# Kernel optimization log

Measured on AMD Instinct MI355X. Metric: run time of the kernel, lower is better.

## Reference

```python
import jax, jax.numpy as jnp
import numpy as np

# ---- constants ----
RC = 6.0            # radial cutoff for Bessel basis
SQ2 = 1.4142135623730951
SQ3 = 1.7320508075688772
SQ6 = 2.449489742783178
CY2 = 2.7386127875258306  # sqrt(15/2), l=2 spherical-harmonic norm
G, N_NODES, N_EDGES = 4, 4096, 65536
NB, C, NZ = 8, 32, 3

# orthonormal basis of symmetric-traceless 3x3 matrices <-> 5-vector (real l=2)

def t5_from_mat(S):
    r2, r6 = 1.0 / SQ2, 1.0 / SQ6
    a = (S[..., 0, 1] + S[..., 1, 0]) * r2
    b = (S[..., 1, 2] + S[..., 2, 1]) * r2
    c = (2.0 * S[..., 2, 2] - S[..., 0, 0] - S[..., 1, 1]) * r6
    d = (S[..., 0, 2] + S[..., 2, 0]) * r2
    e = (S[..., 0, 0] - S[..., 1, 1]) * r2
    return jnp.stack([a, b, c, d, e], axis=-1)

def mat_from_t5(t):
    r2, r6 = 1.0 / SQ2, 1.0 / SQ6
    a, b, c, d, e = (t[..., i] for i in range(5))
    Sxx = -c * r6 + e * r2
    Syy = -c * r6 - e * r2
    Szz = 2.0 * c * r6
    Sxy, Syz, Sxz = a * r2, b * r2, d * r2
    row0 = jnp.stack([Sxx, Sxy, Sxz], -1)
    row1 = jnp.stack([Sxy, Syy, Syz], -1)
    row2 = jnp.stack([Sxz, Syz, Szz], -1)
    return jnp.stack([row0, row1, row2], -2)

def bessel(r, nbessel):
    # sqrt(2/rc) * sin(n*pi*r/rc) / r, smooth at r=0 via sinc
    n = jnp.arange(1, nbessel + 1, dtype=r.dtype)
    x = r[..., None] * n / RC
    return jnp.sqrt(2.0 / RC) * (n * jnp.pi / RC) * jnp.sinc(x)

def sph(vec):
    # real spherical harmonics l=0,1,2 of the unit edge vector
    u = vec / (jnp.linalg.norm(vec, axis=-1, keepdims=True) + 1e-9)
    Y0 = jnp.ones(u.shape[:-1] + (1,), u.dtype)
    Y1 = SQ3 * u
    outer = u[..., :, None] * u[..., None, :]
    Y2 = CY2 * t5_from_mat(outer - jnp.eye(3, dtype=u.dtype) / 3.0)
    return Y0, Y1, Y2

def message_pass(r, vec, h_scalar, src, dst, Wrad, n_nodes):
    # A_l[n] = sum_{e: dst(e)=n} R(r_e)W_l * h_src[e] * Y_l(v_e)
    R = bessel(r, Wrad.shape[0])                      # [E, nb]
    w = jnp.einsum('eb,bcl->ecl', R, Wrad)            # [E, C, 3]
    Y0, Y1, Y2 = sph(vec)
    hs = h_scalar[src]                                # gather -> [E, C]
    m0 = (w[:, :, 0] * hs)[:, :, None] * Y0[:, None, :]
    m1 = (w[:, :, 1] * hs)[:, :, None] * Y1[:, None, :]
    m2 = (w[:, :, 2] * hs)[:, :, None] * Y2[:, None, :]
    m = jnp.concatenate([m0, m1, m2], axis=-1)        # [E, C, 9]
    A = jax.ops.segment_sum(m, dst, num_segments=n_nodes)
    return A[..., 0], A[..., 1:4], A[..., 4:9]        # [N,C],[N,C,3],[N,C,5]

def prod3body(A0, A1, A2, Wp):
    # symmetric 3-body tensor product A x A with CG paths to 0e+1o+2e
    dot11 = jnp.sum(A1 * A1, -1)
    dot22 = jnp.sum(A2 * A2, -1)
    B0 = Wp[0] * A0 * A0 + Wp[1] * dot11 + Wp[2] * dot22
    T = mat_from_t5(A2)                               # [N,C,3,3]
    Tv = jnp.einsum('ncij,ncj->nci', T, A1)           # 1x2 -> 1 path
    B1 = Wp[3][:, None] * A0[..., None] * A1 + Wp[4][:, None] * Tv
    eye = jnp.eye(3, dtype=A1.dtype)
    S = A1[..., :, None] * A1[..., None, :] - (dot11 / 3.0)[..., None, None] * eye
    B2 = Wp[5][:, None] * A0[..., None] * A2 + Wp[6][:, None] * t5_from_mat(S)
    return B0, B1, B2

def readout_l2(B0, B2, Wr0, Wr2):
    # per-node symmetric 3x3: isotropic scalar part + traceless l=2 part
    s = B0 @ Wr0                                      # [N]
    t = jnp.einsum('ncm,c->nm', B2, Wr2)              # [N,5]
    eye = jnp.eye(3, dtype=B0.dtype)
    return s[:, None, None] * eye / SQ3 + mat_from_t5(t)


def setup_inputs() -> dict:
    key = jax.random.key(0)
    ks = jax.random.split(key, 14)
    sc = 1.0 / np.sqrt(C)
    return {
        'x': jax.random.uniform(ks[0], (G, N_EDGES), jnp.float32),
        'x_v': jax.random.normal(ks[1], (G, N_EDGES, 3), jnp.float32),
        'node_attr': jax.random.uniform(ks[2], (G, N_NODES, NZ), jnp.float32),
        'edge_index': jax.random.randint(ks[3], (G, 2, N_EDGES), 0, N_NODES),
        'Wz': jax.random.normal(ks[4], (NZ, C), jnp.float32) * 0.5,
        'Wrad1': jax.random.normal(ks[5], (NB, C, 3), jnp.float32) * 0.5,
        'Wrad2': jax.random.normal(ks[6], (NB, C, 3), jnp.float32) * 0.5,
        'Wp': jax.random.normal(ks[7], (7, C), jnp.float32) * 0.5,
        'Wr0_1': jax.random.normal(ks[8], (C,), jnp.float32) * sc,
        'Wr2_1': jax.random.normal(ks[9], (C,), jnp.float32) * sc,
        'Wm0': jax.random.normal(ks[10], (C, C), jnp.float32) * sc,
        'Wr0_2': jax.random.normal(ks[11], (C,), jnp.float32) * sc,
        'Wr2_2': jax.random.normal(ks[12], (C,), jnp.float32) * sc,
    }


def reference(x, x_v, node_attr, edge_index, Wz, Wrad1, Wrad2, Wp,
              Wr0_1, Wr2_1, Wm0, Wr0_2, Wr2_2):
    n_nodes = node_attr.shape[1]

    def per_graph(r, vec, na, ei):
        src, dst = ei[0], ei[1]
        h0 = na @ Wz                                  # NodeFeaturesStart
        A0, A1, A2 = message_pass(r, vec, h0, src, dst, Wrad1, n_nodes)
        B0, B1, B2 = prod3body(A0, A1, A2, Wp)
        M1 = readout_l2(B0, B2, Wr0_1, Wr2_1)         # [N,3,3]
        f0 = jax.nn.silu(B0 @ Wm0)                    # updated node scalars
        A0b, A1b, A2b = message_pass(r, vec, f0, src, dst, Wrad2, n_nodes)
        C0, C1, C2b = prod3body(A0b, A1b, A2b, Wp)    # prod reused (as in torch code)
        M2 = readout_l2(C0, C2b, Wr0_2, Wr2_2)
        return M1.sum(0) + M2.sum(0)                  # [3,3]

    return jax.vmap(per_graph)(x, x_v, node_attr, edge_index)
```

## Files before the change

### kernel.cpp

```cpp
#include <hip/hip_runtime.h>
#include <hip/hip_fp16.h>
#include <math.h>

#define G_ 4
#define N_ 4096
#define E_ 65536
#define NB_ 8
#define C_ 32
#define CAP_ 48

typedef _Float16 h2 __attribute__((ext_vector_type(2)));

__device__ __forceinline__ float red32(float v) {
    #pragma unroll
    for (int o = 16; o >= 1; o >>= 1) v += __shfl_xor(v, o, 32);
    return v;
}

__device__ __forceinline__ float pack2f(float a, float b) {
    union { __half2 h; unsigned u; } cvt;
    cvt.h = __floats2half2_rn(a, b);
    return __uint_as_float(cvt.u);
}

__device__ __forceinline__ unsigned pack2u(float a, float b) {
    union { __half2 h; unsigned u; } cvt;
    cvt.h = __floats2half2_rn(a, b);
    return cvt.u;
}

__device__ __forceinline__ h2 as_h2(float fbits) {
    union { float f; h2 h; } u; u.f = fbits; return u.h;
}

__device__ __forceinline__ h2 as_h2u(unsigned ubits) {
    union { unsigned u; h2 h; } u2; u2.u = ubits; return u2.h;
}

__global__ void k_prep(const float* __restrict__ x, const float* __restrict__ xv,
                       const int* __restrict__ ei, const float* __restrict__ na,
                       const float* __restrict__ Wz, const float* __restrict__ Wrad1,
                       const float* __restrict__ Wrad2, int* __restrict__ cur,
                       float4* __restrict__ rec32, float* __restrict__ h,
                       unsigned* __restrict__ Wpk) {
    int idx = blockIdx.x * 256 + threadIdx.x;

    if (blockIdx.x == 0 && threadIdx.x < 192) {
        int t = threadIdx.x;
        int pass = t / 96, rem = t % 96;
        int c = rem / 3, l = rem % 3;
        const float* W = pass ? Wrad2 : Wrad1;
        unsigned* dst = Wpk + ((size_t)(pass * C_ + c) * 3 + l) * 4;
        #pragma unroll
        for (int j = 0; j < 4; ++j)
            dst[j] = pack2u(W[(2 * j) * (C_ * 3) + c * 3 + l],
                            W[(2 * j + 1) * (C_ * 3) + c * 3 + l]);
    }

    #pragma unroll
    for (int t = 0; t < 2; ++t) {
        int hidx = idx + t * (G_ * E_);
        int c = hidx & (C_ - 1), gn = hidx >> 5;
        const float* a = na + (size_t)gn * 3;
        h[hidx] = a[0] * Wz[c] + a[1] * Wz[C_ + c] + a[2] * Wz[2 * C_ + c];
    }

    int g = idx >> 16, e = idx & (E_ - 1);
    const int* eib = ei + (size_t)g * 2 * E_;
    int src = eib[e], dst = eib[E_ + e];
    int local = atomicAdd(&cur[g * N_ + dst], 1);
    if (local >= CAP_) return;
    size_t slot = (size_t)(g * N_ + dst) * CAP_ + local;

    float r = x[idx];
    const float SQ2RC = 0.57735026918962576f;
    const float K1 = 0.5235987755982988f;
    float rinv = (r > 1e-12f) ? (1.0f / r) : 0.0f;
    bool  tiny = (r <= 1e-12f);
    float xx = K1 * r;
    float s1, c1;
    __sincosf(xx, &s1, &c1);
    float twoc = 2.0f * c1;
    float R[NB_];
    float sm = 0.f, sn = s1;
    #pragma unroll
    for (int n = 1; n <= NB_; ++n) {
        R[n - 1] = tiny ? (SQ2RC * K1 * (float)n) : (SQ2RC * sn * rinv);
        float nx = twoc * sn - sm;
        sm = sn; sn = nx;
    }

    float ax = xv[(size_t)idx * 3 + 0];
    float ay = xv[(size_t)idx * 3 + 1];
    float az = xv[(size_t)idx * 3 + 2];
    float inr = 1.7320508075688772f * rsqrtf(ax * ax + ay * ay + az * az + 1e-18f);

    float4* p = rec32 + slot * 2;
    p[0] = make_float4(ax * inr, ay * inr, az * inr, __int_as_float(src));
    p[1] = make_float4(pack2f(R[0], R[1]), pack2f(R[2], R[3]),
                       pack2f(R[4], R[5]), pack2f(R[6], R[7]));
}

template <int PASS>
__global__ void __launch_bounds__(256) k_node(
        const float4* __restrict__ rec32, const int* __restrict__ cur,
        const float* __restrict__ hin, const unsigned* __restrict__ Wpk,
        const float* __restrict__ Wp, const float* __restrict__ Wr0,
        const float* __restrict__ Wr2, const float* __restrict__ Wm0,
        float* __restrict__ f0out, float* __restrict__ pacc) {
    __shared__ float4 sbin[4][CAP_ * 2];
    __shared__ float  sred[6][4][32];
    int tid  = threadIdx.x;
    int wv   = tid >> 6;
    int lane = tid & 63;
    int c    = lane & 31;
    int eo   = lane >> 5;
    int gn   = blockIdx.x * 4 + wv;
    int g    = gn >> 12;

    const uint4* wp = (const uint4*)(Wpk + (size_t)((PASS - 1) * C_ + c) * 12);
    uint4 wq0 = wp[0], wq1 = wp[1], wq2 = wp[2];

    int deg = cur[gn];
    if (deg > CAP_) deg = CAP_;
    {
        const float4* bin = rec32 + (size_t)gn * CAP_ * 2;
        int nf4 = deg * 2;
        for (int j = lane; j < nf4; j += 64) sbin[wv][j] = bin[j];
    }
    __syncthreads();

    h2 wh[3][4];
    wh[0][0] = as_h2u(wq0.x); wh[0][1] = as_h2u(wq0.y);
    wh[0][2] = as_h2u(wq0.z); wh[0][3] = as_h2u(wq0.w);
    wh[1][0] = as_h2u(wq1.x); wh[1][1] = as_h2u(wq1.y);
    wh[1][2] = as_h2u(wq1.z); wh[1][3] = as_h2u(wq1.w);
    wh[2][0] = as_h2u(wq2.x); wh[2][1] = as_h2u(wq2.y);
    wh[2][2] = as_h2u(wq2.z); wh[2][3] = as_h2u(wq2.w);

    const float* hbase = hin + (size_t)g * N_ * C_;

    float A0 = 0, A1x = 0, A1y = 0, A1z = 0;
    float A20 = 0, A21 = 0, A22 = 0, A23 = 0, A24 = 0;

    const float CA = 1.2909944487358056f;
    const float CB = 0.37267799624996495f;
    const float CC = 0.6454972243679028f;

    int M = (deg - eo + 1) >> 1;
    if (deg <= eo) M = 0;

    auto pre_h = [&](int i) -> float {
        int s = eo + 2 * i;
        if (s >= deg) return 0.f;
        int src = __float_as_int(sbin[wv][2 * s].w);
        return hbase[(size_t)src * C_ + c];
    };
    auto do_slot = [&](int i, float hs) {
        int s = eo + 2 * i;
        if (s < deg) {
            float4 r0 = sbin[wv][2 * s];
            float4 r1 = sbin[wv][2 * s + 1];
            h2 Rh0 = as_h2(r1.x), Rh1 = as_h2(r1.y), Rh2 = as_h2(r1.z), Rh3 = as_h2(r1.w);
            float w0 = __builtin_amdgcn_fdot2(Rh3, wh[0][3],
                       __builtin_amdgcn_fdot2(Rh2, wh[0][2],
                       __builtin_amdgcn_fdot2(Rh1, wh[0][1],
                       __builtin_amdgcn_fdot2(Rh0, wh[0][0], 0.f, false), false), false), false);
            float w1 = __builtin_amdgcn_fdot2(Rh3, wh[1][3],
                       __builtin_amdgcn_fdot2(Rh2, wh[1][2],
                       __builtin_amdgcn_fdot2(Rh1, wh[1][1],
                       __builtin_amdgcn_fdot2(Rh0, wh[1][0], 0.f, false), false), false), false);
            float w2 = __builtin_amdgcn_fdot2(Rh3, wh[2][3],
                       __builtin_amdgcn_fdot2(Rh2, wh[2][2],
                       __builtin_amdgcn_fdot2(Rh1, wh[2][1],
                       __builtin_amdgcn_fdot2(Rh0, wh[2][0], 0.f, false), false), false), false);
            float m0 = w0 * hs, m1 = w1 * hs, m2 = w2 * hs;
            float vx = r0.x, vy = r0.y, vz = r0.z;
            A0  += m0;
            A1x += m1 * vx; A1y += m1 * vy; A1z += m1 * vz;
            float pxy = vx * vy, pyz = vy * vz, pxz = vx * vz;
            float pxx = vx * vx, pyy = vy * vy, pzz = vz * vz;
            float m2a = m2 * CA;
            A20 += m2a * pxy;
            A21 += m2a * pyz;
            A22 += (m2 * CB) * (2.0f * pzz - pxx - pyy);
            A23 += m2a * pxz;
            A24 += (m2 * CC) * (pxx - pyy);
        }
    };

    float hp0 = pre_h(0), hp1 = pre_h(1), hp2 = pre_h(2), hp3 = pre_h(3);
    for (int i = 0; i < M; i += 4) {
        float n0 = pre_h(i + 4), n1 = pre_h(i + 5), n2 = pre_h(i + 6), n3 = pre_h(i + 7);
        do_slot(i, hp0);
        do_slot(i + 1, hp1);
        do_slot(i + 2, hp2);
        do_slot(i + 3, hp3);
        hp0 = n0; hp1 = n1; hp2 = n2; hp3 = n3;
    }

    A0  += __shfl_xor(A0, 32);
    A1x += __shfl_xor(A1x, 32);
    A1y += __shfl_xor(A1y, 32);
    A1z += __shfl_xor(A1z, 32);
    A20 += __shfl_xor(A20, 32);
    A21 += __shfl_xor(A21, 32);
    A22 += __shfl_xor(A22, 32);
    A23 += __shfl_xor(A23, 32);
    A24 += __shfl_xor(A24, 32);

    float d11 = A1x * A1x + A1y * A1y + A1z * A1z;
    float d22 = A20 * A20 + A21 * A21 + A22 * A22 + A23 * A23 + A24 * A24;
    float B0 = Wp[0 * C_ + c] * A0 * A0 + Wp[1 * C_ + c] * d11 + Wp[2 * C_ + c] * d22;

    float w5 = Wp[5 * C_ + c], w6 = Wp[6 * C_ + c];
    const float S2  = 1.4142135623730951f;
    const float IS6 = 0.4082482904638631f;
    const float IS2 = 0.7071067811865476f;
    float B20 = w5 * A0 * A20 + w6 * (S2 * A1x * A1y);
    float B21 = w5 * A0 * A21 + w6 * (S2 * A1y * A1z);
    float B22 = w5 * A0 * A22 + w6 * ((2.0f * A1z * A1z - A1x * A1x - A1y * A1y) * IS6);
    float B23 = w5 * A0 * A23 + w6 * (S2 * A1x * A1z);
    float B24 = w5 * A0 * A24 + w6 * ((A1x * A1x - A1y * A1y) * IS2);

    if (eo == 0) {
        float wr0 = Wr0[c], wr2 = Wr2[c];
        sred[0][wv][c] = B0  * wr0;
        sred[1][wv][c] = B20 * wr2;
        sred[2][wv][c] = B21 * wr2;
        sred[3][wv][c] = B22 * wr2;
        sred[4][wv][c] = B23 * wr2;
        sred[5][wv][c] = B24 * wr2;
    }

    if (PASS == 1) {
        float sum = 0.f;
        int k0 = eo << 4;
        #pragma unroll
        for (int k = 0; k < 16; ++k)
            sum += __shfl(B0, k0 + k, 32) * Wm0[(k0 + k) * C_ + c];
        sum += __shfl_xor(sum, 32);
        float sig = 1.0f / (1.0f + __expf(-sum));
        if (eo == 0) f0out[(size_t)gn * C_ + c] = sum * sig;
    }

    __syncthreads();
    if (tid < 192) {
        int i = tid >> 5, cc = tid & 31;
        float s = sred[i][0][cc] + sred[i][1][cc] + sred[i][2][cc] + sred[i][3][cc];
        s = red32(s);
        if (cc == 0) pacc[(size_t)blockIdx.x * 6 + i] = s;
    }
}

__global__ void k_final(const float* __restrict__ pacc1, const float* __restrict__ pacc2,
                        float* __restrict__ out) {
    int t = threadIdx.x;
    int g = t >> 6, lane = t & 63;
    const int BPG = N_ / 4;
    float v[6] = {0, 0, 0, 0, 0, 0};
    for (int b = lane; b < BPG; b += 64) {
        const float* p1 = pacc1 + (size_t)(g * BPG + b) * 6;
        const float* p2 = pacc2 + (size_t)(g * BPG + b) * 6;
        #pragma unroll
        for (int i = 0; i < 6; ++i) v[i] += p1[i] + p2[i];
    }
    #pragma unroll
    for (int i = 0; i < 6; ++i) {
        #pragma unroll
        for (int o = 32; o >= 1; o >>= 1) v[i] += __shfl_xor(v[i], o, 64);
    }
    if (lane == 0) {
        const float IS3 = 0.5773502691896258f;
        const float IS6 = 0.4082482904638631f;
        const float IS2 = 0.7071067811865476f;
        float diag = v[0] * IS3;
        float Sxx = -v[3] * IS6 + v[5] * IS2 + diag;
        float Syy = -v[3] * IS6 - v[5] * IS2 + diag;
        float Szz = 2.0f * v[3] * IS6 + diag;
        float Sxy = v[1] * IS2, Syz = v[2] * IS2, Sxz = v[4] * IS2;
        float* o = out + g * 9;
        o[0] = Sxx; o[1] = Sxy; o[2] = Sxz;
        o[3] = Sxy; o[4] = Syy; o[5] = Syz;
        o[6] = Sxz; o[7] = Syz; o[8] = Szz;
    }
}

extern "C" void kernel_launch(void* const* d_in, const int* in_sizes, int n_in,
                              void* d_out, int out_size, void* d_ws, size_t ws_size,
                              hipStream_t stream) {
    const float* x     = (const float*)d_in[0];
    const float* xv    = (const float*)d_in[1];
    const float* na    = (const float*)d_in[2];
    const int*   ei    = (const int*)d_in[3];
    const float* Wz    = (const float*)d_in[4];
    const float* Wrad1 = (const float*)d_in[5];
    const float* Wrad2 = (const float*)d_in[6];
    const float* Wp    = (const float*)d_in[7];
    const float* Wr0_1 = (const float*)d_in[8];
    const float* Wr2_1 = (const float*)d_in[9];
    const float* Wm0   = (const float*)d_in[10];
    const float* Wr0_2 = (const float*)d_in[11];
    const float* Wr2_2 = (const float*)d_in[12];
    float* out = (float*)d_out;

    float* ws = (float*)d_ws;
    const size_t REC_FL = (size_t)G_ * N_ * CAP_ * 8;
    const size_t H_FL   = (size_t)G_ * N_ * C_;
    const int    NBLK   = G_ * N_ / 4;
    float4*   rec32 = (float4*)ws;
    float*    h     = ws + REC_FL;
    float*    f0    = h + H_FL;
    int*      cur   = (int*)(f0 + H_FL);
    float*    pacc1 = (float*)(cur + G_ * N_);
    float*    pacc2 = pacc1 + (size_t)NBLK * 6;
    unsigned* Wpk   = (unsigned*)(pacc2 + (size_t)NBLK * 6);

    hipMemsetAsync(cur, 0, G_ * N_ * sizeof(int), stream);

    k_prep<<<(G_ * E_) / 256, 256, 0, stream>>>(x, xv, ei, na, Wz, Wrad1, Wrad2,
                                                cur, rec32, h, Wpk);

    k_node<1><<<NBLK, 256, 0, stream>>>(rec32, cur, h,  Wpk, Wp,
                                        Wr0_1, Wr2_1, Wm0, f0, pacc1);
    k_node<2><<<NBLK, 256, 0, stream>>>(rec32, cur, f0, Wpk, Wp,
                                        Wr0_2, Wr2_2, nullptr, nullptr, pacc2);

    k_final<<<1, 256, 0, stream>>>(pacc1, pacc2, out);
}
```

Before: 149.4 us.

## Process two nodes per wavefront and reduce partials per wave without block sync

Each wavefront now handles two consecutive nodes. It loads both nodes' edge bins into its own shared-memory slice and accumulates the readout contributions in registers, so the block-level shared-memory reduction and both __syncthreads are gone. Each wave reduces its partials with shuffles and writes one 6-float record. The grid is halved, the weight loads are amortized over two nodes, and k_final reads twice as many per-wave partials. The trade-off is less parallelism: the two nodes are processed one after the other within a wave, with more shared memory per block.

```diff
diff --git a/kernel.cpp b/kernel.cpp
--- a/kernel.cpp
+++ b/kernel.cpp
@@ -108,27 +108,31 @@
         const float* __restrict__ Wp, const float* __restrict__ Wr0,
         const float* __restrict__ Wr2, const float* __restrict__ Wm0,
         float* __restrict__ f0out, float* __restrict__ pacc) {
-    __shared__ float4 sbin[4][CAP_ * 2];
-    __shared__ float  sred[6][4][32];
+    __shared__ float4 sbin[4][2][CAP_ * 2];
     int tid  = threadIdx.x;
     int wv   = tid >> 6;
     int lane = tid & 63;
     int c    = lane & 31;
     int eo   = lane >> 5;
-    int gn   = blockIdx.x * 4 + wv;
-    int g    = gn >> 12;
+    int wid  = blockIdx.x * 4 + wv;
+    int gn0  = wid * 2;
+    int g    = gn0 >> 12;
 
     const uint4* wp = (const uint4*)(Wpk + (size_t)((PASS - 1) * C_ + c) * 12);
     uint4 wq0 = wp[0], wq1 = wp[1], wq2 = wp[2];
 
-    int deg = cur[gn];
-    if (deg > CAP_) deg = CAP_;
+    int2 dg = *(const int2*)(cur + gn0);
+    int deg0 = dg.x > CAP_ ? CAP_ : dg.x;
+    int deg1 = dg.y > CAP_ ? CAP_ : dg.y;
+
     {
-        const float4* bin = rec32 + (size_t)gn * CAP_ * 2;
-        int nf4 = deg * 2;
-        for (int j = lane; j < nf4; j += 64) sbin[wv][j] = bin[j];
-    }
-    __syncthreads();
+        const float4* bin0 = rec32 + (size_t)gn0 * CAP_ * 2;
+        int nf0 = deg0 * 2, nft = nf0 + deg1 * 2;
+        for (int j = lane; j < nft; j += 64) {
+            if (j < nf0) sbin[wv][0][j] = bin0[j];
+            else         sbin[wv][1][j - nf0] = bin0[CAP_ * 2 + (j - nf0)];
+        }
+    }
 
     h2 wh[3][4];
     wh[0][0] = as_h2u(wq0.x); wh[0][1] = as_h2u(wq0.y);
@@ -139,129 +143,135 @@
     wh[2][2] = as_h2u(wq2.z); wh[2][3] = as_h2u(wq2.w);
 
     const float* hbase = hin + (size_t)g * N_ * C_;
-
-    float A0 = 0, A1x = 0, A1y = 0, A1z = 0;
-    float A20 = 0, A21 = 0, A22 = 0, A23 = 0, A24 = 0;
-
     const float CA = 1.2909944487358056f;
     const float CB = 0.37267799624996495f;
     const float CC = 0.6454972243679028f;
-
-    int M = (deg - eo + 1) >> 1;
-    if (deg <= eo) M = 0;
-
-    auto pre_h = [&](int i) -> float {
-        int s = eo + 2 * i;
-        if (s >= deg) return 0.f;
-        int src = __float_as_int(sbin[wv][2 * s].w);
-        return hbase[(size_t)src * C_ + c];
-    };
-    auto do_slot = [&](int i, float hs) {
-        int s = eo + 2 * i;
-        if (s < deg) {
-            float4 r0 = sbin[wv][2 * s];
-            float4 r1 = sbin[wv][2 * s + 1];
-            h2 Rh0 = as_h2(r1.x), Rh1 = as_h2(r1.y), Rh2 = as_h2(r1.z), Rh3 = as_h2(r1.w);
-            float w0 = __builtin_amdgcn_fdot2(Rh3, wh[0][3],
-                       __builtin_amdgcn_fdot2(Rh2, wh[0][2],
-                       __builtin_amdgcn_fdot2(Rh1, wh[0][1],
-                       __builtin_amdgcn_fdot2(Rh0, wh[0][0], 0.f, false), false), false), false);
-            float w1 = __builtin_amdgcn_fdot2(Rh3, wh[1][3],
-                       __builtin_amdgcn_fdot2(Rh2, wh[1][2],
-                       __builtin_amdgcn_fdot2(Rh1, wh[1][1],
-                       __builtin_amdgcn_fdot2(Rh0, wh[1][0], 0.f, false), false), false), false);
-            float w2 = __builtin_amdgcn_fdot2(Rh3, wh[2][3],
-                       __builtin_amdgcn_fdot2(Rh2, wh[2][2],
-                       __builtin_amdgcn_fdot2(Rh1, wh[2][1],
-                       __builtin_amdgcn_fdot2(Rh0, wh[2][0], 0.f, false), false), false), false);
-            float m0 = w0 * hs, m1 = w1 * hs, m2 = w2 * hs;
-            float vx = r0.x, vy = r0.y, vz = r0.z;
-            A0  += m0;
-            A1x += m1 * vx; A1y += m1 * vy; A1z += m1 * vz;
-            float pxy = vx * vy, pyz = vy * vz, pxz = vx * vz;
-            float pxx = vx * vx, pyy = vy * vy, pzz = vz * vz;
-            float m2a = m2 * CA;
-            A20 += m2a * pxy;
-            A21 += m2a * pyz;
-            A22 += (m2 * CB) * (2.0f * pzz - pxx - pyy);
-            A23 += m2a * pxz;
-            A24 += (m2 * CC) * (pxx - pyy);
-        }
-    };
-
-    float hp0 = pre_h(0), hp1 = pre_h(1), hp2 = pre_h(2), hp3 = pre_h(3);
-    for (int i = 0; i < M; i += 4) {
-        float n0 = pre_h(i + 4), n1 = pre_h(i + 5), n2 = pre_h(i + 6), n3 = pre_h(i + 7);
-        do_slot(i, hp0);
-        do_slot(i + 1, hp1);
-        do_slot(i + 2, hp2);
-        do_slot(i + 3, hp3);
-        hp0 = n0; hp1 = n1; hp2 = n2; hp3 = n3;
-    }
-
-    A0  += __shfl_xor(A0, 32);
-    A1x += __shfl_xor(A1x, 32);
-    A1y += __shfl_xor(A1y, 32);
-    A1z += __shfl_xor(A1z, 32);
-    A20 += __shfl_xor(A20, 32);
-    A21 += __shfl_xor(A21, 32);
-    A22 += __shfl_xor(A22, 32);
-    A23 += __shfl_xor(A23, 32);
-    A24 += __shfl_xor(A24, 32);
-
-    float d11 = A1x * A1x + A1y * A1y + A1z * A1z;
-    float d22 = A20 * A20 + A21 * A21 + A22 * A22 + A23 * A23 + A24 * A24;
-    float B0 = Wp[0 * C_ + c] * A0 * A0 + Wp[1 * C_ + c] * d11 + Wp[2 * C_ + c] * d22;
-
-    float w5 = Wp[5 * C_ + c], w6 = Wp[6 * C_ + c];
     const float S2  = 1.4142135623730951f;
     const float IS6 = 0.4082482904638631f;
     const float IS2 = 0.7071067811865476f;
-    float B20 = w5 * A0 * A20 + w6 * (S2 * A1x * A1y);
-    float B21 = w5 * A0 * A21 + w6 * (S2 * A1y * A1z);
-    float B22 = w5 * A0 * A22 + w6 * ((2.0f * A1z * A1z - A1x * A1x - A1y * A1y) * IS6);
-    float B23 = w5 * A0 * A23 + w6 * (S2 * A1x * A1z);
-    float B24 = w5 * A0 * A24 + w6 * ((A1x * A1x - A1y * A1y) * IS2);
-
-    if (eo == 0) {
-        float wr0 = Wr0[c], wr2 = Wr2[c];
-        sred[0][wv][c] = B0  * wr0;
-        sred[1][wv][c] = B20 * wr2;
-        sred[2][wv][c] = B21 * wr2;
-        sred[3][wv][c] = B22 * wr2;
-        sred[4][wv][c] = B23 * wr2;
-        sred[5][wv][c] = B24 * wr2;
-    }
-
-    if (PASS == 1) {
-        float sum = 0.f;
-        int k0 = eo << 4;
-        #pragma unroll
-        for (int k = 0; k < 16; ++k)
-            sum += __shfl(B0, k0 + k, 32) * Wm0[(k0 + k) * C_ + c];
-        sum += __shfl_xor(sum, 32);
-        float sig = 1.0f / (1.0f + __expf(-sum));
-        if (eo == 0) f0out[(size_t)gn * C_ + c] = sum * sig;
-    }
-
-    __syncthreads();
-    if (tid < 192) {
-        int i = tid >> 5, cc = tid & 31;
-        float s = sred[i][0][cc] + sred[i][1][cc] + sred[i][2][cc] + sred[i][3][cc];
-        s = red32(s);
-        if (cc == 0) pacc[(size_t)blockIdx.x * 6 + i] = s;
-    }
+    float wr0 = Wr0[c], wr2 = Wr2[c];
+    float wp0 = Wp[0 * C_ + c], wp1 = Wp[1 * C_ + c], wp2 = Wp[2 * C_ + c];
+    float w5  = Wp[5 * C_ + c], w6  = Wp[6 * C_ + c];
+
+    float racc[6] = {0.f, 0.f, 0.f, 0.f, 0.f, 0.f};
+
+    #pragma unroll
+    for (int nd = 0; nd < 2; ++nd) {
+        int deg = nd ? deg1 : deg0;
+        float A0 = 0, A1x = 0, A1y = 0, A1z = 0;
+        float A20 = 0, A21 = 0, A22 = 0, A23 = 0, A24 = 0;
+
+        int M = (deg - eo + 1) >> 1;
+        if (deg <= eo) M = 0;
+
+        auto pre_h = [&](int i) -> float {
+            int s = eo + 2 * i;
+            if (s >= deg) return 0.f;
+            int src = __float_as_int(sbin[wv][nd][2 * s].w);
+            return hbase[(size_t)src * C_ + c];
+        };
+        auto do_slot = [&](int i, float hs) {
+            int s = eo + 2 * i;
+            if (s < deg) {
+                float4 r0 = sbin[wv][nd][2 * s];
+                float4 r1 = sbin[wv][nd][2 * s + 1];
+                h2 Rh0 = as_h2(r1.x), Rh1 = as_h2(r1.y), Rh2 = as_h2(r1.z), Rh3 = as_h2(r1.w);
+                float w0 = __builtin_amdgcn_fdot2(Rh3, wh[0][3],
+                           __builtin_amdgcn_fdot2(Rh2, wh[0][2],
+                           __builtin_amdgcn_fdot2(Rh1, wh[0][1],
+                           __builtin_amdgcn_fdot2(Rh0, wh[0][0], 0.f, false), false), false), false);
+                float w1 = __builtin_amdgcn_fdot2(Rh3, wh[1][3],
+                           __builtin_amdgcn_fdot2(Rh2, wh[1][2],
+                           __builtin_amdgcn_fdot2(Rh1, wh[1][1],
+                           __builtin_amdgcn_fdot2(Rh0, wh[1][0], 0.f, false), false), false), false);
+                float w2 = __builtin_amdgcn_fdot2(Rh3, wh[2][3],
+                           __builtin_amdgcn_fdot2(Rh2, wh[2][2],
+                           __builtin_amdgcn_fdot2(Rh1, wh[2][1],
+                           __builtin_amdgcn_fdot2(Rh0, wh[2][0], 0.f, false), false), false), false);
+                float m0 = w0 * hs, m1 = w1 * hs, m2 = w2 * hs;
+                float vx = r0.x, vy = r0.y, vz = r0.z;
+                A0  += m0;
+                A1x += m1 * vx; A1y += m1 * vy; A1z += m1 * vz;
+                float pxy = vx * vy, pyz = vy * vz, pxz = vx * vz;
+                float pxx = vx * vx, pyy = vy * vy, pzz = vz * vz;
+                float m2a = m2 * CA;
+                A20 += m2a * pxy;
+                A21 += m2a * pyz;
+                A22 += (m2 * CB) * (2.0f * pzz - pxx - pyy);
+                A23 += m2a * pxz;
+                A24 += (m2 * CC) * (pxx - pyy);
+            }
+        };
+
+        float hp0 = pre_h(0), hp1 = pre_h(1), hp2 = pre_h(2), hp3 = pre_h(3);
+        for (int i = 0; i < M; i += 4) {
+            float n0 = pre_h(i + 4), n1 = pre_h(i + 5), n2 = pre_h(i + 6), n3 = pre_h(i + 7);
+            do_slot(i, hp0);
+            do_slot(i + 1, hp1);
+            do_slot(i + 2, hp2);
+            do_slot(i + 3, hp3);
+            hp0 = n0; hp1 = n1; hp2 = n2; hp3 = n3;
+        }
+
+        A0  += __shfl_xor(A0, 32);
+        A1x += __shfl_xor(A1x, 32);
+        A1y += __shfl_xor(A1y, 32);
+        A1z += __shfl_xor(A1z, 32);
+        A20 += __shfl_xor(A20, 32);
+        A21 += __shfl_xor(A21, 32);
+        A22 += __shfl_xor(A22, 32);
+        A23 += __shfl_xor(A23, 32);
+        A24 += __shfl_xor(A24, 32);
+
+        float d11 = A1x * A1x + A1y * A1y + A1z * A1z;
+        float d22 = A20 * A20 + A21 * A21 + A22 * A22 + A23 * A23 + A24 * A24;
+        float B0 = wp0 * A0 * A0 + wp1 * d11 + wp2 * d22;
+
+        float B20 = w5 * A0 * A20 + w6 * (S2 * A1x * A1y);
+        float B21 = w5 * A0 * A21 + w6 * (S2 * A1y * A1z);
+        float B22 = w5 * A0 * A22 + w6 * ((2.0f * A1z * A1z - A1x * A1x - A1y * A1y) * IS6);
+        float B23 = w5 * A0 * A23 + w6 * (S2 * A1x * A1z);
+        float B24 = w5 * A0 * A24 + w6 * ((A1x * A1x - A1y * A1y) * IS2);
+
+        racc[0] += B0  * wr0;
+        racc[1] += B20 * wr2;
+        racc[2] += B21 * wr2;
+        racc[3] += B22 * wr2;
+        racc[4] += B23 * wr2;
+        racc[5] += B24 * wr2;
+
+        if (PASS == 1) {
+            float sum = 0.f;
+            int k0 = eo << 4;
+            #pragma unroll
+            for (int k = 0; k < 16; ++k)
+                sum += __shfl(B0, k0 + k, 32) * Wm0[(k0 + k) * C_ + c];
+            sum += __shfl_xor(sum, 32);
+            float sig = 1.0f / (1.0f + __expf(-sum));
+            if (eo == 0) f0out[(size_t)(gn0 + nd) * C_ + c] = sum * sig;
+        }
+    }
+
+    float r0 = red32(racc[0]);
+    float r1 = red32(racc[1]);
+    float r2 = red32(racc[2]);
+    float r3 = red32(racc[3]);
+    float r4 = red32(racc[4]);
+    float r5 = red32(racc[5]);
+    float v = (lane == 0) ? r0 : (lane == 1) ? r1 : (lane == 2) ? r2
+            : (lane == 3) ? r3 : (lane == 4) ? r4 : r5;
+    if (lane < 6) pacc[(size_t)wid * 6 + lane] = v;
 }
 
 __global__ void k_final(const float* __restrict__ pacc1, const float* __restrict__ pacc2,
                         float* __restrict__ out) {
     int t = threadIdx.x;
     int g = t >> 6, lane = t & 63;
-    const int BPG = N_ / 4;
+    const int WPG = (N_ / 2);
     float v[6] = {0, 0, 0, 0, 0, 0};
-    for (int b = lane; b < BPG; b += 64) {
-        const float* p1 = pacc1 + (size_t)(g * BPG + b) * 6;
-        const float* p2 = pacc2 + (size_t)(g * BPG + b) * 6;
+    for (int b = lane; b < WPG; b += 64) {
+        const float* p1 = pacc1 + (size_t)(g * WPG + b) * 6;
+        const float* p2 = pacc2 + (size_t)(g * WPG + b) * 6;
         #pragma unroll
         for (int i = 0; i < 6; ++i) v[i] += p1[i] + p2[i];
     }
@@ -307,24 +317,24 @@
     float* ws = (float*)d_ws;
     const size_t REC_FL = (size_t)G_ * N_ * CAP_ * 8;
     const size_t H_FL   = (size_t)G_ * N_ * C_;
-    const int    NBLK   = G_ * N_ / 4;
+    const int    NWAVE  = G_ * N_ / 2;
     float4*   rec32 = (float4*)ws;
     float*    h     = ws + REC_FL;
     float*    f0    = h + H_FL;
     int*      cur   = (int*)(f0 + H_FL);
     float*    pacc1 = (float*)(cur + G_ * N_);
-    float*    pacc2 = pacc1 + (size_t)NBLK * 6;
-    unsigned* Wpk   = (unsigned*)(pacc2 + (size_t)NBLK * 6);
+    float*    pacc2 = pacc1 + (size_t)NWAVE * 6;
+    unsigned* Wpk   = (unsigned*)(pacc2 + (size_t)NWAVE * 6);
 
     hipMemsetAsync(cur, 0, G_ * N_ * sizeof(int), stream);
 
     k_prep<<<(G_ * E_) / 256, 256, 0, stream>>>(x, xv, ei, na, Wz, Wrad1, Wrad2,
                                                 cur, rec32, h, Wpk);
 
-    k_node<1><<<NBLK, 256, 0, stream>>>(rec32, cur, h,  Wpk, Wp,
-                                        Wr0_1, Wr2_1, Wm0, f0, pacc1);
-    k_node<2><<<NBLK, 256, 0, stream>>>(rec32, cur, f0, Wpk, Wp,
-                                        Wr0_2, Wr2_2, nullptr, nullptr, pacc2);
+    k_node<1><<<NWAVE / 4, 256, 0, stream>>>(rec32, cur, h,  Wpk, Wp,
+                                             Wr0_1, Wr2_1, Wm0, f0, pacc1);
+    k_node<2><<<NWAVE / 4, 256, 0, stream>>>(rec32, cur, f0, Wpk, Wp,
+                                             Wr0_2, Wr2_2, nullptr, nullptr, pacc2);
 
     k_final<<<1, 256, 0, stream>>>(pacc1, pacc2, out);
 }
```

New measurement: 160.6 us. 1.07x slower.
